# Performance work log

Hardware: AMD Instinct MI355X
Metric: run time of the kernel (lower is better)

## Reference

```python
import jax, jax.numpy as jnp
import numpy as np

B, S, OUT = 128, 3000, 84
CODE_SEQ = 30
LAT = 1024
C, D = 128, 16
CB = C * D  # 2048
IN = CODE_SEQ * OUT  # 2520


def setup_inputs() -> dict:
    key = jax.random.key(0)
    ks = jax.random.split(key, 16)
    def w(k, shape):
        fan_in = shape[0]
        return (jax.random.normal(k, shape, dtype=jnp.float32) / np.sqrt(fan_in)).astype(jnp.float32)
    return {
        "y": jax.random.normal(ks[0], (B, S, OUT), dtype=jnp.float32),
        "emb": jax.random.uniform(ks[1], (C, D), minval=-1.0 / C, maxval=1.0 / C, dtype=jnp.float32),
        "eW1": w(ks[2], (IN, LAT)), "eb1": jnp.zeros((LAT,), jnp.float32),
        "eW2": w(ks[3], (LAT, LAT)), "eb2": jnp.zeros((LAT,), jnp.float32),
        "eW3": w(ks[4], (LAT, CB)), "eb3": jnp.zeros((CB,), jnp.float32),
        "dW1": w(ks[5], (CB, LAT)), "db1": jnp.zeros((LAT,), jnp.float32),
        "dW2": w(ks[6], (LAT, LAT)), "db2": jnp.zeros((LAT,), jnp.float32),
        "dW3": w(ks[7], (LAT, IN)), "db3": jnp.zeros((IN,), jnp.float32),
    }


def _mlp(z, W1, b1, W2, b2, W3, b3):
    # LinearEncoder in eval mode (dropout = identity): Linear->ELU->Linear->ELU->Linear
    z = jax.nn.elu(z @ W1 + b1)
    z = jax.nn.elu(z @ W2 + b2)
    return z @ W3 + b3


def reference(y, emb, eW1, eb1, eW2, eb2, eW3, eb3, dW1, db1, dW2, db2, dW3, db3):
    batch, seq_len = y.shape[0], y.shape[1]
    # seq_len % code_seq == 0 -> padding branch is a no-op
    y2 = y.reshape(batch, -1, IN)                 # (B, n_m, 2520)
    n_m = y2.shape[1]
    ze = _mlp(y2, eW1, eb1, eW2, eb2, eW3, eb3)   # (B, n_m, 2048)
    zef = ze.reshape(batch, n_m, -1, D)           # (B, n_m, G=128, 16)
    # squared L2 distance to each of C codes, without materializing (B,n_m,G,C,D)
    dist = (
        jnp.sum(zef ** 2, -1, keepdims=True)
        - 2.0 * jnp.einsum("bngd,cd->bngc", zef, emb)
        + jnp.sum(emb ** 2, -1)
    )                                             # (B, n_m, G, C)
    nn_idx = jnp.argmin(dist, -1)                 # (B, n_m, G)
    zq = emb[nn_idx].reshape(batch, n_m, -1)      # (B, n_m, 2048)
    dec_in = ze + jax.lax.stop_gradient(zq - ze)  # straight-through
    out = _mlp(dec_in, dW1, db1, dW2, db2, dW3, db3)
    out = out.reshape(batch, -1, OUT)[:, :seq_len, :]
    return (out, ze, zq)
```

## Files before the change

### kernel.cpp

```cpp
#include <hip/hip_runtime.h>
#include <hip/hip_bf16.h>
#include <cstdint>
#include <cstddef>

typedef __bf16 bf16_t;
typedef bf16_t bf16x8 __attribute__((ext_vector_type(8)));
typedef float  f32x4  __attribute__((ext_vector_type(4)));

__device__ __forceinline__ void gl_lds16(const void* g, void* l) {
  __builtin_amdgcn_global_load_lds(
      (const __attribute__((address_space(1))) void*)g,
      (__attribute__((address_space(3))) void*)l, 16, 0, 0);
}

#define BAR()  __builtin_amdgcn_s_barrier()

__device__ __forceinline__ void transpose_tile(
    const float* __restrict__ W, bf16_t* __restrict__ Wt,
    int K, int N, int Kpad, int Npad, int bx, int by, int t)
{
  __shared__ float tile[32][33];
  const int tx = t & 31, ty = t >> 5;
  const int k0 = bx * 32, n0 = by * 32;
#pragma unroll
  for (int i = 0; i < 4; ++i) {
    int k = k0 + ty + i * 8, n = n0 + tx;
    tile[ty + i * 8][tx] = (k < K && n < N) ? W[(size_t)k * N + n] : 0.f;
  }
  __syncthreads();
#pragma unroll
  for (int i = 0; i < 4; ++i) {
    int n = n0 + ty + i * 8, k = k0 + tx;
    if (n < Npad && k < Kpad)
      Wt[(size_t)n * Kpad + k] = (bf16_t)tile[tx][ty + i * 8];
  }
}

__global__ __launch_bounds__(256) void prep_kernel(
    const float* __restrict__ y, bf16_t* __restrict__ X0,
    const float* __restrict__ eW1, bf16_t* __restrict__ W1t,
    const float* __restrict__ eW2, bf16_t* __restrict__ W2t,
    const float* __restrict__ eW3, bf16_t* __restrict__ W3t,
    const float* __restrict__ dW1, bf16_t* __restrict__ V1t,
    const float* __restrict__ dW2, bf16_t* __restrict__ V2t,
    const float* __restrict__ dW3, bf16_t* __restrict__ V3t)
{
  const int b = blockIdx.x;
  const int t = threadIdx.x;
  if (b < 16000) {
    const int idx = b * 256 + t;
    const int r = idx / 320, c = (idx % 320) * 8;
    bf16x8 v;
    if (c < 2520) {
      const float4 f0 = *(const float4*)(y + (size_t)r * 2520 + c);
      const float4 f1 = *(const float4*)(y + (size_t)r * 2520 + c + 4);
      v[0] = (bf16_t)f0.x; v[1] = (bf16_t)f0.y; v[2] = (bf16_t)f0.z; v[3] = (bf16_t)f0.w;
      v[4] = (bf16_t)f1.x; v[5] = (bf16_t)f1.y; v[6] = (bf16_t)f1.z; v[7] = (bf16_t)f1.w;
    } else {
#pragma unroll
      for (int j = 0; j < 8; ++j) v[j] = (bf16_t)0.f;
    }
    *(bf16x8*)(X0 + (size_t)r * 2560 + c) = v;
    return;
  }
  int lb = b - 16000;
  if (lb < 2560)      { transpose_tile(eW1, W1t, 2520, 1024, 2560, 1024, lb % 80, lb / 80, t); return; }
  lb -= 2560;
  if (lb < 1024)      { transpose_tile(eW2, W2t, 1024, 1024, 1024, 1024, lb % 32, lb / 32, t); return; }
  lb -= 1024;
  if (lb < 2048)      { transpose_tile(eW3, W3t, 1024, 2048, 1024, 2048, lb % 32, lb / 32, t); return; }
  lb -= 2048;
  if (lb < 2048)      { transpose_tile(dW1, V1t, 2048, 1024, 2048, 1024, lb % 64, lb / 64, t); return; }
  lb -= 2048;
  if (lb < 1024)      { transpose_tile(dW2, V2t, 1024, 1024, 1024, 1024, lb % 32, lb / 32, t); return; }
  lb -= 1024;
  transpose_tile(dW3, V3t, 1024, 2520, 1024, 2560, lb % 32, lb / 32, t);
}

template<int ELU>
__global__ __launch_bounds__(512, 4) void gemm128(
    const bf16_t* __restrict__ A, const bf16_t* __restrict__ Bt,
    const float* __restrict__ bias,
    bf16_t* __restrict__ Cb, float* __restrict__ Cf,
    int M, int N, int K, int Nlog)
{
  __shared__ __align__(16) bf16_t lds[36864];

  const int t  = threadIdx.x;
  const int w  = t >> 6, l = t & 63;
  const int fr = l & 15, kg = l >> 4;
  const int wm = (w >> 1) * 64, wn = (w & 1) * 64;

  const int gx = gridDim.x;
  const int nwg = gx * (int)gridDim.y;
  int lin = blockIdx.y * gx + blockIdx.x;
  int q8 = nwg >> 3, r8 = nwg & 7, xcd = lin & 7, idx = lin >> 3;
  int swz = (xcd < r8 ? xcd * (q8 + 1) : r8 * (q8 + 1) + (xcd - r8) * q8) + idx;
  const int tn = (swz % gx) * 128;
  const int tm = (swz / gx) * 256;

  const int srow = t >> 2;
  const int scol = (t & 3) * 8;
  const int sdst = t * 8;

  const int NT = K >> 5;

  f32x4 acc[4][4];
#pragma unroll
  for (int i = 0; i < 4; ++i)
#pragma unroll
    for (int j = 0; j < 4; ++j) acc[i][j] = (f32x4){0.f, 0.f, 0.f, 0.f};

  auto stage = [&](int slot, int kn) {
    bf16_t* d = lds + slot * 12288;
    gl_lds16(A  + (size_t)(tm + srow) * K + kn + scol,       d + sdst);
    gl_lds16(A  + (size_t)(tm + 128 + srow) * K + kn + scol, d + 4096 + sdst);
    gl_lds16(Bt + (size_t)(tn + srow) * K + kn + scol,       d + 8192 + sdst);
  };

  stage(0, 0);
  stage(1, 32);
  asm volatile("s_waitcnt vmcnt(3)" ::: "memory");
  BAR();

  for (int kt = 0; kt < NT; ++kt) {
    const int slot = kt % 3;
    const bf16_t* aH = lds + slot * 12288 + wm * 32;
    const bf16_t* bH = lds + slot * 12288 + 8192 + wn * 32;

    if (kt + 2 < NT) stage((kt + 2) % 3, (kt + 2) << 5);

    bf16x8 af[4], bf_[4];
#pragma unroll
    for (int q = 0; q < 4; ++q) {
      af[q]  = *(const bf16x8*)(aH + (q * 16 + fr) * 32 + kg * 8);
      bf_[q] = *(const bf16x8*)(bH + (q * 16 + fr) * 32 + kg * 8);
    }
    __builtin_amdgcn_s_setprio(1);
#pragma unroll
    for (int mi = 0; mi < 4; ++mi)
#pragma unroll
      for (int nj = 0; nj < 4; ++nj)
        acc[mi][nj] = __builtin_amdgcn_mfma_f32_16x16x32_bf16(af[mi], bf_[nj], acc[mi][nj], 0, 0, 0);
    __builtin_amdgcn_s_setprio(0);

    if (kt + 2 < NT) {
      asm volatile("s_waitcnt vmcnt(3)" ::: "memory");
    } else if (kt + 1 < NT) {
      asm volatile("s_waitcnt vmcnt(0)" ::: "memory");
    }
    BAR();
  }

#pragma unroll
  for (int mi = 0; mi < 4; ++mi) {
    const int row0 = tm + wm + mi * 16 + kg * 4;
#pragma unroll
    for (int nj = 0; nj < 4; ++nj) {
      const int col = tn + wn + nj * 16 + fr;
      const float bv = (col < Nlog) ? bias[col] : 0.f;
#pragma unroll
      for (int r = 0; r < 4; ++r) {
        float v = acc[mi][nj][r] + bv;
        if (ELU) v = (v > 0.f) ? v : expm1f(v);
        const int row = row0 + r;
        if (Cb) Cb[(size_t)row * N + col] = (bf16_t)v;
        if (Cf && col < Nlog) Cf[(size_t)row * Nlog + col] = v;
      }
    }
  }
}

__global__ __launch_bounds__(256) void vq_mfma(
    const float* __restrict__ ze, const float* __restrict__ emb,
    float* __restrict__ zq, bf16_t* __restrict__ zqb)
{
  __shared__ float  se[2048];
  __shared__ bf16_t seb[2048];
  const int t = threadIdx.x;
  for (int i = t; i < 2048; i += 256) { float v = emb[i]; se[i] = v; seb[i] = (bf16_t)v; }
  __syncthreads();

  const int l = t & 63, w = t >> 6;
  const int col = l & 15;
  const int ks8 = (l >> 4) * 8;
  const bool kact = (ks8 < 16);

  bf16x8 bfrag[8];
  float  hv[8];
#pragma unroll
  for (int cb = 0; cb < 8; ++cb) {
    float s = 0.f;
    bf16x8 bf;
#pragma unroll
    for (int j = 0; j < 8; ++j) bf[j] = (bf16_t)0.f;
    if (kact) {
      const float* ep = se + (cb * 16 + col) * 16 + ks8;
      float4 e0 = *(const float4*)ep;
      float4 e1 = *(const float4*)(ep + 4);
      bf[0] = (bf16_t)e0.x; bf[1] = (bf16_t)e0.y; bf[2] = (bf16_t)e0.z; bf[3] = (bf16_t)e0.w;
      bf[4] = (bf16_t)e1.x; bf[5] = (bf16_t)e1.y; bf[6] = (bf16_t)e1.z; bf[7] = (bf16_t)e1.w;
      s = e0.x*e0.x + e0.y*e0.y + e0.z*e0.z + e0.w*e0.w
        + e1.x*e1.x + e1.y*e1.y + e1.z*e1.z + e1.w*e1.w;
    }
    s += __shfl_xor(s, 16);
    s += __shfl_xor(s, 32);
    bfrag[cb] = bf;
    hv[cb] = 0.5f * s;
  }

  const int base_tile = blockIdx.x * 64 + w * 16;
  for (int it = 0; it < 16; ++it) {
    const int tile = base_tile + it;
    const int row = tile >> 3, g0 = (tile & 7) * 16;

    bf16x8 afrag;
#pragma unroll
    for (int j = 0; j < 8; ++j) afrag[j] = (bf16_t)0.f;
    if (kact) {
      const float* ap = ze + (size_t)row * 2048 + (g0 + col) * 16 + ks8;
      float4 a0 = *(const float4*)ap;
      float4 a1 = *(const float4*)(ap + 4);
      afrag[0] = (bf16_t)(-a0.x); afrag[1] = (bf16_t)(-a0.y);
      afrag[2] = (bf16_t)(-a0.z); afrag[3] = (bf16_t)(-a0.w);
      afrag[4] = (bf16_t)(-a1.x); afrag[5] = (bf16_t)(-a1.y);
      afrag[6] = (bf16_t)(-a1.z); afrag[7] = (bf16_t)(-a1.w);
    }

    f32x4 dd[8];
#pragma unroll
    for (int cb = 0; cb < 8; ++cb) {
      f32x4 c = (f32x4){hv[cb], hv[cb], hv[cb], hv[cb]};
      dd[cb] = __builtin_amdgcn_mfma_f32_16x16x32_bf16(afrag, bfrag[cb], c, 0, 0, 0);
    }

#pragma unroll
    for (int r = 0; r < 4; ++r) {
      float bd = dd[0][r]; int bi = col;
#pragma unroll
      for (int cb = 1; cb < 8; ++cb) {
        float v = dd[cb][r];
        int   ci = cb * 16 + col;
        if (v < bd) { bd = v; bi = ci; }
      }
#pragma unroll
      for (int m = 1; m < 16; m <<= 1) {
        float od = __shfl_xor(bd, m);
        int   oi = __shfl_xor(bi, m);
        if (od < bd || (od == bd && oi < bi)) { bd = od; bi = oi; }
      }
      if (col == r) {
        const int tok = (l >> 4) * 4 + r;
        const size_t go = ((size_t)row * 128 + g0 + tok) * 16;
        const float*  e  = se  + bi * 16;
        const bf16_t* eb = seb + bi * 16;
#pragma unroll
        for (int v = 0; v < 4; ++v)
          *(float4*)(zq + go + v * 4) = ((const float4*)e)[v];
        *(bf16x8*)(zqb + go)     = ((const bf16x8*)eb)[0];
        *(bf16x8*)(zqb + go + 8) = ((const bf16x8*)eb)[1];
      }
    }
  }
}

extern "C" void kernel_launch(void* const* d_in, const int* in_sizes, int n_in,
                              void* d_out, int out_size, void* d_ws, size_t ws_size,
                              hipStream_t stream)
{
  const float* y   = (const float*)d_in[0];
  const float* emb = (const float*)d_in[1];
  const float* eW1 = (const float*)d_in[2];
  const float* eb1 = (const float*)d_in[3];
  const float* eW2 = (const float*)d_in[4];
  const float* eb2 = (const float*)d_in[5];
  const float* eW3 = (const float*)d_in[6];
  const float* eb3 = (const float*)d_in[7];
  const float* dW1 = (const float*)d_in[8];
  const float* db1 = (const float*)d_in[9];
  const float* dW2 = (const float*)d_in[10];
  const float* db2 = (const float*)d_in[11];
  const float* dW3 = (const float*)d_in[12];
  const float* db3 = (const float*)d_in[13];

  float* out = (float*)d_out;
  float* ze  = out + 32256000;
  float* zq  = ze + 26214400;

  uint8_t* ws = (uint8_t*)d_ws;
  size_t off = 0;
  auto alloc = [&](size_t bytes) -> void* {
    void* p = ws + off; off += (bytes + 255) & ~(size_t)255; return p;
  };
  bf16_t* X0  = (bf16_t*)alloc(12800ULL * 2560 * 2);
  bf16_t* W1t = (bf16_t*)alloc(1024ULL * 2560 * 2);
  bf16_t* W2t = (bf16_t*)alloc(1024ULL * 1024 * 2);
  bf16_t* W3t = (bf16_t*)alloc(2048ULL * 1024 * 2);
  bf16_t* V1t = (bf16_t*)alloc(1024ULL * 2048 * 2);
  bf16_t* V2t = (bf16_t*)alloc(1024ULL * 1024 * 2);
  bf16_t* V3t = (bf16_t*)alloc(2560ULL * 1024 * 2);
  bf16_t* H1  = (bf16_t*)alloc(12800ULL * 1024 * 2);
  bf16_t* H2  = (bf16_t*)alloc(12800ULL * 1024 * 2);
  bf16_t* ZQb = (bf16_t*)alloc(12800ULL * 2048 * 2);

  prep_kernel<<<27264, 256, 0, stream>>>(y, X0, eW1, W1t, eW2, W2t, eW3, W3t,
                                         dW1, V1t, dW2, V2t, dW3, V3t);

  gemm128<1><<<dim3(8, 50), 512, 0, stream>>>(X0, W1t, eb1, H1, nullptr, 12800, 1024, 2560, 1024);
  gemm128<1><<<dim3(8, 50), 512, 0, stream>>>(H1, W2t, eb2, H2, nullptr, 12800, 1024, 1024, 1024);
  gemm128<0><<<dim3(16, 50), 512, 0, stream>>>(H2, W3t, eb3, nullptr, ze, 12800, 2048, 1024, 2048);
  vq_mfma<<<1600, 256, 0, stream>>>(ze, emb, zq, ZQb);
  gemm128<1><<<dim3(8, 50), 512, 0, stream>>>(ZQb, V1t, db1, H1, nullptr, 12800, 1024, 2048, 1024);
  gemm128<1><<<dim3(8, 50), 512, 0, stream>>>(H1, V2t, db2, H2, nullptr, 12800, 1024, 1024, 1024);
  gemm128<0><<<dim3(20, 50), 512, 0, stream>>>(H2, V3t, db3, nullptr, out, 12800, 2560, 1024, 2520);
}
```

Measured before the change: 612.0 us.

## Fuse VQ nearest-code search into the encoder's final GEMM epilogue

Replaces the separate third encoder GEMM and vq_mfma kernel with one gemm_vq kernel. After the K loop it writes ze, stages each wave's accumulator tile in LDS, then runs the MFMA-based distance and argmin from there, writing zq and the bf16 zq. This avoids re-reading the fp32 ze buffer from global memory and saves one launch. In exchange the GEMM epilogue gets heavier and uses more registers and LDS, which may lower occupancy. zq is now rebuilt from bf16-rounded codebook values rather than fp32, a precision change.

Result: slower. 983.6 us (+60.7%).

```diff
diff --git a/kernel.cpp b/kernel.cpp
--- a/kernel.cpp
+++ b/kernel.cpp
@@ -171,94 +171,178 @@
   }
 }
 
-__global__ __launch_bounds__(256) void vq_mfma(
-    const float* __restrict__ ze, const float* __restrict__ emb,
-    float* __restrict__ zq, bf16_t* __restrict__ zqb)
-{
-  __shared__ float  se[2048];
-  __shared__ bf16_t seb[2048];
-  const int t = threadIdx.x;
-  for (int i = t; i < 2048; i += 256) { float v = emb[i]; se[i] = v; seb[i] = (bf16_t)v; }
+__global__ __launch_bounds__(512, 4) void gemm_vq(
+    const bf16_t* __restrict__ A, const bf16_t* __restrict__ Bt,
+    const float* __restrict__ bias, const float* __restrict__ emb,
+    float* __restrict__ ze, float* __restrict__ zq, bf16_t* __restrict__ zqb,
+    int M, int K)
+{
+  __shared__ __align__(16) bf16_t lds[36864];
+
+  const int t  = threadIdx.x;
+  const int w  = t >> 6, l = t & 63;
+  const int fr = l & 15, kg = l >> 4;
+  const int wm = (w >> 1) * 64, wn = (w & 1) * 64;
+
+  const int gx = gridDim.x;
+  const int nwg = gx * (int)gridDim.y;
+  int lin = blockIdx.y * gx + blockIdx.x;
+  int q8 = nwg >> 3, r8 = nwg & 7, xcd = lin & 7, idx = lin >> 3;
+  int swz = (xcd < r8 ? xcd * (q8 + 1) : r8 * (q8 + 1) + (xcd - r8) * q8) + idx;
+  const int tn = (swz % gx) * 128;
+  const int tm = (swz / gx) * 256;
+
+  const int srow = t >> 2;
+  const int scol = (t & 3) * 8;
+  const int sdst = t * 8;
+
+  const int NT = K >> 5;
+
+  f32x4 acc[4][4];
+#pragma unroll
+  for (int i = 0; i < 4; ++i)
+#pragma unroll
+    for (int j = 0; j < 4; ++j) acc[i][j] = (f32x4){0.f, 0.f, 0.f, 0.f};
+
+  auto stage = [&](int slot, int kn) {
+    bf16_t* d = lds + slot * 12288;
+    gl_lds16(A  + (size_t)(tm + srow) * K + kn + scol,       d + sdst);
+    gl_lds16(A  + (size_t)(tm + 128 + srow) * K + kn + scol, d + 4096 + sdst);
+    gl_lds16(Bt + (size_t)(tn + srow) * K + kn + scol,       d + 8192 + sdst);
+  };
+
+  stage(0, 0);
+  stage(1, 32);
+  asm volatile("s_waitcnt vmcnt(3)" ::: "memory");
+  BAR();
+
+  for (int kt = 0; kt < NT; ++kt) {
+    const int slot = kt % 3;
+    const bf16_t* aH = lds + slot * 12288 + wm * 32;
+    const bf16_t* bH = lds + slot * 12288 + 8192 + wn * 32;
+
+    if (kt + 2 < NT) stage((kt + 2) % 3, (kt + 2) << 5);
+
+    bf16x8 af[4], bf_[4];
+#pragma unroll
+    for (int q = 0; q < 4; ++q) {
+      af[q]  = *(const bf16x8*)(aH + (q * 16 + fr) * 32 + kg * 8);
+      bf_[q] = *(const bf16x8*)(bH + (q * 16 + fr) * 32 + kg * 8);
+    }
+    __builtin_amdgcn_s_setprio(1);
+#pragma unroll
+    for (int mi = 0; mi < 4; ++mi)
+#pragma unroll
+      for (int nj = 0; nj < 4; ++nj)
+        acc[mi][nj] = __builtin_amdgcn_mfma_f32_16x16x32_bf16(af[mi], bf_[nj], acc[mi][nj], 0, 0, 0);
+    __builtin_amdgcn_s_setprio(0);
+
+    if (kt + 2 < NT) {
+      asm volatile("s_waitcnt vmcnt(3)" ::: "memory");
+    } else if (kt + 1 < NT) {
+      asm volatile("s_waitcnt vmcnt(0)" ::: "memory");
+    }
+    BAR();
+  }
+
+  bf16_t* seb = lds;
+  float*  wF  = (float*)((char*)lds + 4096 + w * 8704);
+
+  for (int i = t; i < 2048; i += 512) seb[i] = (bf16_t)emb[i];
   __syncthreads();
 
-  const int l = t & 63, w = t >> 6;
-  const int col = l & 15;
-  const int ks8 = (l >> 4) * 8;
+  const int col = fr;
+  const int ks8 = kg * 8;
   const bool kact = (ks8 < 16);
 
+  float hv[8];
   bf16x8 bfrag[8];
-  float  hv[8];
 #pragma unroll
   for (int cb = 0; cb < 8; ++cb) {
+    const float* ep = emb + (cb * 16 + col) * 16;
     float s = 0.f;
+#pragma unroll
+    for (int j = 0; j < 16; ++j) s += ep[j] * ep[j];
+    hv[cb] = 0.5f * s;
     bf16x8 bf;
 #pragma unroll
     for (int j = 0; j < 8; ++j) bf[j] = (bf16_t)0.f;
-    if (kact) {
-      const float* ep = se + (cb * 16 + col) * 16 + ks8;
-      float4 e0 = *(const float4*)ep;
-      float4 e1 = *(const float4*)(ep + 4);
-      bf[0] = (bf16_t)e0.x; bf[1] = (bf16_t)e0.y; bf[2] = (bf16_t)e0.z; bf[3] = (bf16_t)e0.w;
-      bf[4] = (bf16_t)e1.x; bf[5] = (bf16_t)e1.y; bf[6] = (bf16_t)e1.z; bf[7] = (bf16_t)e1.w;
-      s = e0.x*e0.x + e0.y*e0.y + e0.z*e0.z + e0.w*e0.w
-        + e1.x*e1.x + e1.y*e1.y + e1.z*e1.z + e1.w*e1.w;
-    }
-    s += __shfl_xor(s, 16);
-    s += __shfl_xor(s, 32);
+    if (kact) bf = *(const bf16x8*)(seb + (cb * 16 + col) * 16 + ks8);
     bfrag[cb] = bf;
-    hv[cb] = 0.5f * s;
-  }
-
-  const int base_tile = blockIdx.x * 64 + w * 16;
-  for (int it = 0; it < 16; ++it) {
-    const int tile = base_tile + it;
-    const int row = tile >> 3, g0 = (tile & 7) * 16;
-
-    bf16x8 afrag;
-#pragma unroll
-    for (int j = 0; j < 8; ++j) afrag[j] = (bf16_t)0.f;
-    if (kact) {
-      const float* ap = ze + (size_t)row * 2048 + (g0 + col) * 16 + ks8;
-      float4 a0 = *(const float4*)ap;
-      float4 a1 = *(const float4*)(ap + 4);
-      afrag[0] = (bf16_t)(-a0.x); afrag[1] = (bf16_t)(-a0.y);
-      afrag[2] = (bf16_t)(-a0.z); afrag[3] = (bf16_t)(-a0.w);
-      afrag[4] = (bf16_t)(-a1.x); afrag[5] = (bf16_t)(-a1.y);
-      afrag[6] = (bf16_t)(-a1.z); afrag[7] = (bf16_t)(-a1.w);
-    }
-
-    f32x4 dd[8];
-#pragma unroll
-    for (int cb = 0; cb < 8; ++cb) {
-      f32x4 c = (f32x4){hv[cb], hv[cb], hv[cb], hv[cb]};
-      dd[cb] = __builtin_amdgcn_mfma_f32_16x16x32_bf16(afrag, bfrag[cb], c, 0, 0, 0);
-    }
-
-#pragma unroll
-    for (int r = 0; r < 4; ++r) {
-      float bd = dd[0][r]; int bi = col;
-#pragma unroll
-      for (int cb = 1; cb < 8; ++cb) {
-        float v = dd[cb][r];
-        int   ci = cb * 16 + col;
-        if (v < bd) { bd = v; bi = ci; }
-      }
-#pragma unroll
-      for (int m = 1; m < 16; m <<= 1) {
-        float od = __shfl_xor(bd, m);
-        int   oi = __shfl_xor(bi, m);
-        if (od < bd || (od == bd && oi < bi)) { bd = od; bi = oi; }
-      }
-      if (col == r) {
-        const int tok = (l >> 4) * 4 + r;
-        const size_t go = ((size_t)row * 128 + g0 + tok) * 16;
-        const float*  e  = se  + bi * 16;
-        const bf16_t* eb = seb + bi * 16;
-#pragma unroll
-        for (int v = 0; v < 4; ++v)
-          *(float4*)(zq + go + v * 4) = ((const float4*)e)[v];
-        *(bf16x8*)(zqb + go)     = ((const bf16x8*)eb)[0];
-        *(bf16x8*)(zqb + go + 8) = ((const bf16x8*)eb)[1];
+  }
+
+#pragma unroll
+  for (int h = 0; h < 2; ++h) {
+#pragma unroll
+    for (int mi2 = 0; mi2 < 2; ++mi2) {
+      const int mi = h * 2 + mi2;
+      const int rl0 = mi2 * 16 + kg * 4;
+      const int row0 = tm + wm + mi * 16 + kg * 4;
+#pragma unroll
+      for (int nj = 0; nj < 4; ++nj) {
+        const int cg = tn + wn + nj * 16 + fr;
+        const float bv = bias[cg];
+#pragma unroll
+        for (int r = 0; r < 4; ++r) {
+          const float v = acc[mi][nj][r] + bv;
+          ze[(size_t)(row0 + r) * 2048 + cg] = v;
+          wF[(rl0 + r) * 68 + nj * 16 + fr] = v;
+        }
+      }
+    }
+    asm volatile("s_waitcnt lgkmcnt(0)" ::: "memory");
+
+    for (int ti = 0; ti < 8; ++ti) {
+      bf16x8 afrag;
+#pragma unroll
+      for (int j = 0; j < 8; ++j) afrag[j] = (bf16_t)0.f;
+      if (kact) {
+        const float* ap = wF + (ti * 4 + (col >> 2)) * 68 + (col & 3) * 16 + ks8;
+        float4 a0 = *(const float4*)ap;
+        float4 a1 = *(const float4*)(ap + 4);
+        afrag[0] = (bf16_t)(-a0.x); afrag[1] = (bf16_t)(-a0.y);
+        afrag[2] = (bf16_t)(-a0.z); afrag[3] = (bf16_t)(-a0.w);
+        afrag[4] = (bf16_t)(-a1.x); afrag[5] = (bf16_t)(-a1.y);
+        afrag[6] = (bf16_t)(-a1.z); afrag[7] = (bf16_t)(-a1.w);
+      }
+
+      f32x4 dd[8];
+#pragma unroll
+      for (int cb = 0; cb < 8; ++cb) {
+        f32x4 c = (f32x4){hv[cb], hv[cb], hv[cb], hv[cb]};
+        dd[cb] = __builtin_amdgcn_mfma_f32_16x16x32_bf16(afrag, bfrag[cb], c, 0, 0, 0);
+      }
+
+#pragma unroll
+      for (int r2 = 0; r2 < 4; ++r2) {
+        float bd = dd[0][r2]; int bi = col;
+#pragma unroll
+        for (int cb = 1; cb < 8; ++cb) {
+          float v = dd[cb][r2];
+          int   ci = cb * 16 + col;
+          if (v < bd) { bd = v; bi = ci; }
+        }
+#pragma unroll
+        for (int m = 1; m < 16; m <<= 1) {
+          float od = __shfl_xor(bd, m);
+          int   oi = __shfl_xor(bi, m);
+          if (od < bd || (od == bd && oi < bi)) { bd = od; bi = oi; }
+        }
+        if (col == r2) {
+          const int pair = (l >> 4) * 4 + r2;
+          const size_t rg = (size_t)(tm + wm + h * 32 + ti * 4 + (pair >> 2));
+          const size_t off = rg * 2048 + (tn + wn + (pair & 3) * 16);
+          const bf16_t* eb = seb + bi * 16;
+#pragma unroll
+          for (int v4 = 0; v4 < 4; ++v4) {
+            float4 f;
+            f.x = (float)eb[v4 * 4 + 0]; f.y = (float)eb[v4 * 4 + 1];
+            f.z = (float)eb[v4 * 4 + 2]; f.w = (float)eb[v4 * 4 + 3];
+            *(float4*)(zq + off + v4 * 4) = f;
+          }
+          *(bf16x8*)(zqb + off)     = ((const bf16x8*)eb)[0];
+          *(bf16x8*)(zqb + off + 8) = ((const bf16x8*)eb)[1];
+        }
       }
     }
   }
@@ -308,8 +392,7 @@
 
   gemm128<1><<<dim3(8, 50), 512, 0, stream>>>(X0, W1t, eb1, H1, nullptr, 12800, 1024, 2560, 1024);
   gemm128<1><<<dim3(8, 50), 512, 0, stream>>>(H1, W2t, eb2, H2, nullptr, 12800, 1024, 1024, 1024);
-  gemm128<0><<<dim3(16, 50), 512, 0, stream>>>(H2, W3t, eb3, nullptr, ze, 12800, 2048, 1024, 2048);
-  vq_mfma<<<1600, 256, 0, stream>>>(ze, emb, zq, ZQb);
+  gemm_vq<<<dim3(16, 50), 512, 0, stream>>>(H2, W3t, eb3, emb, ze, zq, ZQb, 12800, 1024);
   gemm128<1><<<dim3(8, 50), 512, 0, stream>>>(ZQb, V1t, db1, H1, nullptr, 12800, 1024, 2048, 1024);
   gemm128<1><<<dim3(8, 50), 512, 0, stream>>>(H1, V2t, db2, H2, nullptr, 12800, 1024, 1024, 1024);
   gemm128<0><<<dim3(20, 50), 512, 0, stream>>>(H2, V3t, db3, nullptr, out, 12800, 2560, 1024, 2520);
```
